# Kernel tuning notes

Measured on AMD Instinct MI355X. Metric: run time of the kernel, lower is better.

Reference implementation:

```python
import jax, jax.numpy as jnp
import numpy as np

B = 32            # decode batch (N flat tokens, q_len=1 each)
D_MODEL = 4096
H = 32            # query heads
HKV = 8           # kv heads (GQA)
HD = 128          # head dim
KVLEN = 2048      # context length per sequence
BLOCK = 256       # paged-cache block size
NBPS = KVLEN // BLOCK          # blocks per sequence = 8
NBLOCKS = B * NBPS             # 256
NSLOTS = NBLOCKS * BLOCK       # 65536
EPS = 1e-6
THETA = 10000.0
NEG = -1e30


def setup_inputs() -> dict:
    key = jax.random.key(0)
    ks = jax.random.split(key, 8)
    seqs = jax.random.normal(ks[0], (B, D_MODEL), dtype=jnp.float32)
    Wq = jax.random.normal(ks[1], (D_MODEL, H * HD), dtype=jnp.float32) * 0.02
    Wk = jax.random.normal(ks[2], (D_MODEL, HKV * HD), dtype=jnp.float32) * 0.02
    Wv = jax.random.normal(ks[3], (D_MODEL, HKV * HD), dtype=jnp.float32) * 0.02
    Wo = jax.random.normal(ks[4], (H * HD, D_MODEL), dtype=jnp.float32) * 0.02
    qn_w = jnp.ones((HD,), dtype=jnp.float32)
    kn_w = jnp.ones((HD,), dtype=jnp.float32)
    k_cache = jax.random.normal(ks[5], (NSLOTS, HKV, HD), dtype=jnp.float32) * 0.02
    v_cache = jax.random.normal(ks[6], (NSLOTS, HKV, HD), dtype=jnp.float32) * 0.02
    # decode step: each seq owns NBPS contiguous blocks; new token goes to last slot
    input_pos = jnp.full((B,), KVLEN - 1, dtype=jnp.int32)
    slot_mapping = (jnp.arange(B, dtype=jnp.int32) * NBPS * BLOCK + (KVLEN - 1)).astype(jnp.int32)
    block_tables = jnp.arange(NBLOCKS, dtype=jnp.int32).reshape(B, NBPS)
    context_lens = jnp.full((B,), KVLEN, dtype=jnp.int32)
    return {
        'seqs': seqs, 'Wq': Wq, 'Wk': Wk, 'Wv': Wv, 'Wo': Wo,
        'qn_w': qn_w, 'kn_w': kn_w, 'k_cache': k_cache, 'v_cache': v_cache,
        'input_pos': input_pos, 'slot_mapping': slot_mapping,
        'block_tables': block_tables, 'context_lens': context_lens,
    }


def _rmsnorm(x, w):
    return x * jax.lax.rsqrt(jnp.mean(x * x, axis=-1, keepdims=True) + EPS) * w


def _rope(x, pos):
    # x: [N, heads, HD], pos: [N]
    half = HD // 2
    inv = 1.0 / (THETA ** (jnp.arange(half, dtype=jnp.float32) / half))
    ang = pos.astype(jnp.float32)[:, None] * inv          # [N, half]
    cos = jnp.cos(ang)[:, None, :]
    sin = jnp.sin(ang)[:, None, :]
    x1, x2 = x[..., :half], x[..., half:]
    return jnp.concatenate([x1 * cos - x2 * sin, x2 * cos + x1 * sin], axis=-1)


def reference(seqs, Wq, Wk, Wv, Wo, qn_w, kn_w, k_cache, v_cache,
              input_pos, slot_mapping, block_tables, context_lens):
    # QKV projections (flat token layout, N = B decode tokens)
    q = (seqs @ Wq).reshape(B, H, HD)
    k = (seqs @ Wk).reshape(B, HKV, HD)
    v = (seqs @ Wv).reshape(B, HKV, HD)
    # qk-norm then RoPE
    q = _rmsnorm(q, qn_w)
    k = _rmsnorm(k, kn_w)
    q = _rope(q, input_pos)
    k = _rope(k, input_pos)
    # paged KV-cache store (slot_mapping scatter)
    kc = k_cache.at[slot_mapping].set(k)
    vc = v_cache.at[slot_mapping].set(v)
    # block-table-indexed gather: slots per sequence [B, KVLEN]
    slots = (block_tables[:, :, None] * BLOCK
             + jnp.arange(BLOCK, dtype=jnp.int32)[None, None, :]).reshape(B, -1)
    K = kc[slots]   # [B, L, HKV, HD]
    V = vc[slots]   # [B, L, HKV, HD]
    L = slots.shape[1]
    # GQA attention: group query heads over kv heads
    G = H // HKV
    qg = q.reshape(B, HKV, G, HD)
    scale = 1.0 / jnp.sqrt(jnp.float32(HD))
    scores = jnp.einsum('bkgd,blkd->bkgl', qg, K) * scale   # [B, HKV, G, L]
    valid = jnp.arange(L, dtype=jnp.int32)[None, :] < context_lens[:, None]
    scores = jnp.where(valid[:, None, None, :], scores, NEG)
    p = jax.nn.softmax(scores, axis=-1)
    out = jnp.einsum('bkgl,blkd->bkgd', p, V).reshape(B, H * HD)
    return out @ Wo
```

## Files before the change

kernel.cpp:

```cpp
#include <hip/hip_runtime.h>
#include <hip/hip_bf16.h>
#include <math.h>

#define B_     32
#define DM_    4096
#define H_     32
#define HKV_   8
#define G_     4
#define HD_    128
#define KVLEN_ 2048
#define PBLK_  256
#define NBPS_  8
#define NQKV_  6144
#define KSPLIT_ 16
#define KC_    256

__global__ __launch_bounds__(256) void qkv_gemm(
    const float* __restrict__ seqs, const float* __restrict__ Wq,
    const float* __restrict__ Wk, const float* __restrict__ Wv,
    float* __restrict__ P1) {
  const int tid = threadIdx.x;
  const int nid = blockIdx.x % 24;
  const int kid = blockIdx.x / 24;
  const int k0 = kid * KC_;

  __shared__ __align__(16) float sT[KC_ * 36];
  #pragma unroll
  for (int m = 0; m < 32; ++m)
    sT[tid * 36 + m] = seqs[m * DM_ + k0 + tid];
  __syncthreads();

  const int n = nid * 256 + tid;
  const float* W; int col, ldw;
  if (nid < 16)      { W = Wq; col = n;        ldw = 4096; }
  else if (nid < 20) { W = Wk; col = n - 4096; ldw = 1024; }
  else               { W = Wv; col = n - 5120; ldw = 1024; }

  float acc[32];
  #pragma unroll
  for (int m = 0; m < 32; ++m) acc[m] = 0.f;

  const float* wp = W + (size_t)k0 * ldw + col;
  #pragma unroll 4
  for (int kk = 0; kk < KC_; ++kk) {
    float w = wp[(size_t)kk * ldw];
    const float4* s4 = (const float4*)&sT[kk * 36];
    #pragma unroll
    for (int mq = 0; mq < 8; ++mq) {
      float4 a = s4[mq];
      acc[mq * 4 + 0] = fmaf(a.x, w, acc[mq * 4 + 0]);
      acc[mq * 4 + 1] = fmaf(a.y, w, acc[mq * 4 + 1]);
      acc[mq * 4 + 2] = fmaf(a.z, w, acc[mq * 4 + 2]);
      acc[mq * 4 + 3] = fmaf(a.w, w, acc[mq * 4 + 3]);
    }
  }
  float* o = P1 + (size_t)kid * 32 * NQKV_ + n;
  #pragma unroll
  for (int m = 0; m < 32; ++m) o[(size_t)m * NQKV_] = acc[m];
}

__global__ __launch_bounds__(128) void reduce_norm_rope(
    const float* __restrict__ P1, const float* __restrict__ qn_w,
    const float* __restrict__ kn_w, const int* __restrict__ input_pos,
    float* __restrict__ qf, float* __restrict__ knew, float* __restrict__ vnew) {
  const int b = blockIdx.x / 48;
  const int hh = blockIdx.x % 48;
  const int tid = threadIdx.x;

  int col0, kind;
  if (hh < 32)      { kind = 0; col0 = hh * 128; }
  else if (hh < 40) { kind = 1; col0 = 4096 + (hh - 32) * 128; }
  else              { kind = 2; col0 = 5120 + (hh - 40) * 128; }

  float x = 0.f;
  const float* p = P1 + (size_t)b * NQKV_ + col0 + tid;
  #pragma unroll
  for (int s = 0; s < KSPLIT_; ++s) x += p[(size_t)s * 32 * NQKV_];

  if (kind == 2) {
    vnew[(size_t)b * 1024 + (hh - 40) * 128 + tid] = x;
    return;
  }

  __shared__ float lds[128];
  __shared__ float wred[2];
  float ss = x * x;
  #pragma unroll
  for (int off = 32; off > 0; off >>= 1) ss += __shfl_down(ss, off);
  if ((tid & 63) == 0) wred[tid >> 6] = ss;
  __syncthreads();
  float tot = wred[0] + wred[1];
  float r = rsqrtf(tot * (1.f / 128.f) + 1e-6f);
  const float* wv = (kind == 0) ? qn_w : kn_w;
  x = x * r * wv[tid];

  lds[tid] = x;
  __syncthreads();

  if (tid < 64) {
    float pos = (float)input_pos[b];
    float inv = powf(10000.f, -(float)tid * (1.f / 64.f));
    float ang = pos * inv;
    float c = cosf(ang), s = sinf(ang);
    float x1 = lds[tid], x2 = lds[tid + 64];
    float o1 = x1 * c - x2 * s;
    float o2 = x2 * c + x1 * s;
    float* dst = (kind == 0) ? (qf + (size_t)b * 4096 + hh * 128)
                             : (knew + (size_t)b * 1024 + (hh - 32) * 128);
    dst[tid] = o1;
    dst[tid + 64] = o2;
  }
}

__global__ __launch_bounds__(512) void attn_decode(
    const float* __restrict__ qf, const float* __restrict__ knew,
    const float* __restrict__ vnew, const float* __restrict__ kc,
    const float* __restrict__ vc, const int* __restrict__ block_tables,
    const int* __restrict__ slot_mapping, const int* __restrict__ context_lens,
    float* __restrict__ attn) {
  const int b   = blockIdx.x >> 3;
  const int kv  = blockIdx.x & 7;
  const int tid = threadIdx.x;
  const int lane = tid & 63;
  const int wid  = tid >> 6;
  const int l16  = lane & 15;
  const int gid  = tid >> 4;
  const int d0   = l16 * 8;

  const int ctx   = context_lens[b];
  const int fslot = slot_mapping[b];
  const int* bt   = block_tables + b * NBPS_;

  const float scale = 0.08838834764831845f;
  float q[4][8];
  #pragma unroll
  for (int g = 0; g < 4; ++g) {
    const float4* qp = (const float4*)(qf + ((size_t)b * H_ + kv * G_ + g) * HD_ + d0);
    float4 a = qp[0], c = qp[1];
    q[g][0] = a.x * scale; q[g][1] = a.y * scale; q[g][2] = a.z * scale; q[g][3] = a.w * scale;
    q[g][4] = c.x * scale; q[g][5] = c.y * scale; q[g][6] = c.z * scale; q[g][7] = c.w * scale;
  }

  float mx[4], ls[4], acc[4][8];
  #pragma unroll
  for (int g = 0; g < 4; ++g) {
    mx[g] = -1e30f; ls[g] = 0.f;
    #pragma unroll
    for (int j = 0; j < 8; ++j) acc[g][j] = 0.f;
  }

  for (int l = gid; l < ctx; l += 32) {
    int page = bt[l >> 8];
    int slot = (page << 8) + (l & 255);
    const float *kp, *vp;
    if (slot == fslot) {
      kp = knew + ((size_t)b * HKV_ + kv) * HD_;
      vp = vnew + ((size_t)b * HKV_ + kv) * HD_;
    } else {
      kp = kc + ((size_t)slot * HKV_ + kv) * HD_;
      vp = vc + ((size_t)slot * HKV_ + kv) * HD_;
    }
    float4 k1 = ((const float4*)(kp + d0))[0];
    float4 k2 = ((const float4*)(kp + d0))[1];
    float4 v1 = ((const float4*)(vp + d0))[0];
    float4 v2 = ((const float4*)(vp + d0))[1];
    float kk[8] = {k1.x, k1.y, k1.z, k1.w, k2.x, k2.y, k2.z, k2.w};
    float vv[8] = {v1.x, v1.y, v1.z, v1.w, v2.x, v2.y, v2.z, v2.w};

    float s[4];
    #pragma unroll
    for (int g = 0; g < 4; ++g) {
      float t = 0.f;
      #pragma unroll
      for (int j = 0; j < 8; ++j) t = fmaf(q[g][j], kk[j], t);
      s[g] = t;
    }
    #pragma unroll
    for (int off = 1; off < 16; off <<= 1) {
      #pragma unroll
      for (int g = 0; g < 4; ++g) s[g] += __shfl_xor(s[g], off);
    }
    #pragma unroll
    for (int g = 0; g < 4; ++g) {
      float nm = fmaxf(mx[g], s[g]);
      float corr = __expf(mx[g] - nm);
      float pw = __expf(s[g] - nm);
      mx[g] = nm;
      ls[g] = ls[g] * corr + pw;
      #pragma unroll
      for (int j = 0; j < 8; ++j) acc[g][j] = fmaf(acc[g][j], corr, pw * vv[j]);
    }
  }

  #pragma unroll
  for (int off = 16; off < 64; off <<= 1) {
    #pragma unroll
    for (int g = 0; g < 4; ++g) {
      float mo = __shfl_xor(mx[g], off);
      float lo = __shfl_xor(ls[g], off);
      float nm = fmaxf(mx[g], mo);
      float c1 = __expf(mx[g] - nm);
      float c2 = __expf(mo - nm);
      ls[g] = ls[g] * c1 + lo * c2;
      mx[g] = nm;
      #pragma unroll
      for (int j = 0; j < 8; ++j) {
        float ao = __shfl_xor(acc[g][j], off);
        acc[g][j] = acc[g][j] * c1 + ao * c2;
      }
    }
  }

  __shared__ float rm[8][4], rl[8][4];
  __shared__ __align__(16) float ra[8][4][128];
  if (lane < 16) {
    #pragma unroll
    for (int g = 0; g < 4; ++g) {
      #pragma unroll
      for (int j = 0; j < 8; ++j) ra[wid][g][d0 + j] = acc[g][j];
    }
    if (lane == 0) {
      #pragma unroll
      for (int g = 0; g < 4; ++g) { rm[wid][g] = mx[g]; rl[wid][g] = ls[g]; }
    }
  }
  __syncthreads();

  {
    int g = tid >> 7;
    int d = tid & 127;
    float M = -1e30f;
    #pragma unroll
    for (int w = 0; w < 8; ++w) M = fmaxf(M, rm[w][g]);
    float L = 0.f, A = 0.f;
    #pragma unroll
    for (int w = 0; w < 8; ++w) {
      float c = __expf(rm[w][g] - M);
      L += c * rl[w][g];
      A += c * ra[w][g][d];
    }
    attn[((size_t)b * H_ + kv * G_ + g) * HD_ + d] = A / L;
  }
}

__global__ __launch_bounds__(256) void oproj_gemm(
    const float* __restrict__ A, const float* __restrict__ Wo,
    float* __restrict__ P2) {
  const int tid = threadIdx.x;
  const int nid = blockIdx.x & 15;
  const int kid = blockIdx.x >> 4;
  const int k0 = kid * KC_;

  __shared__ __align__(16) float sT[KC_ * 36];
  #pragma unroll
  for (int m = 0; m < 32; ++m)
    sT[tid * 36 + m] = A[m * 4096 + k0 + tid];
  __syncthreads();

  const int n = nid * 256 + tid;
  float acc[32];
  #pragma unroll
  for (int m = 0; m < 32; ++m) acc[m] = 0.f;

  const float* wp = Wo + (size_t)k0 * 4096 + n;
  #pragma unroll 4
  for (int kk = 0; kk < KC_; ++kk) {
    float w = wp[(size_t)kk * 4096];
    const float4* s4 = (const float4*)&sT[kk * 36];
    #pragma unroll
    for (int mq = 0; mq < 8; ++mq) {
      float4 a = s4[mq];
      acc[mq * 4 + 0] = fmaf(a.x, w, acc[mq * 4 + 0]);
      acc[mq * 4 + 1] = fmaf(a.y, w, acc[mq * 4 + 1]);
      acc[mq * 4 + 2] = fmaf(a.z, w, acc[mq * 4 + 2]);
      acc[mq * 4 + 3] = fmaf(a.w, w, acc[mq * 4 + 3]);
    }
  }
  float* o = P2 + (size_t)kid * 32 * 4096 + n;
  #pragma unroll
  for (int m = 0; m < 32; ++m) o[(size_t)m * 4096] = acc[m];
}

__global__ __launch_bounds__(256) void oproj_reduce(
    const float* __restrict__ P2, float* __restrict__ out) {
  const int idx = blockIdx.x * 256 + threadIdx.x;
  float s = 0.f;
  #pragma unroll
  for (int t = 0; t < KSPLIT_; ++t) s += P2[(size_t)t * 131072 + idx];
  out[idx] = s;
}

extern "C" void kernel_launch(void* const* d_in, const int* in_sizes, int n_in,
                              void* d_out, int out_size, void* d_ws, size_t ws_size,
                              hipStream_t stream) {
  const float* seqs = (const float*)d_in[0];
  const float* Wq   = (const float*)d_in[1];
  const float* Wk   = (const float*)d_in[2];
  const float* Wv   = (const float*)d_in[3];
  const float* Wo   = (const float*)d_in[4];
  const float* qn_w = (const float*)d_in[5];
  const float* kn_w = (const float*)d_in[6];
  const float* kc   = (const float*)d_in[7];
  const float* vc   = (const float*)d_in[8];
  const int* input_pos = (const int*)d_in[9];
  const int* slot_map  = (const int*)d_in[10];
  const int* btab      = (const int*)d_in[11];
  const int* ctx       = (const int*)d_in[12];
  float* out = (float*)d_out;

  char* w = (char*)d_ws;
  float* P1   = (float*)(w);
  float* qf   = (float*)(w + 12582912);
  float* knew = (float*)(w + 13107200);
  float* vnew = (float*)(w + 13238272);
  float* attn = (float*)(w + 13369344);
  float* P2   = (float*)(w + 13893632);

  qkv_gemm<<<24 * KSPLIT_, 256, 0, stream>>>(seqs, Wq, Wk, Wv, P1);
  reduce_norm_rope<<<B_ * 48, 128, 0, stream>>>(P1, qn_w, kn_w, input_pos, qf, knew, vnew);
  attn_decode<<<B_ * HKV_, 512, 0, stream>>>(qf, knew, vnew, kc, vc, btab, slot_map, ctx, attn);
  oproj_gemm<<<16 * KSPLIT_, 256, 0, stream>>>(attn, Wo, P2);
  oproj_reduce<<<512, 256, 0, stream>>>(P2, out);
}
```

Baseline: 228.2 us.

## Split attention over context with max-free softmax merge and widen GEMM column loads

```diff
diff --git a/kernel.cpp b/kernel.cpp
--- a/kernel.cpp
+++ b/kernel.cpp
@@ -9,11 +9,12 @@
 #define G_     4
 #define HD_    128
 #define KVLEN_ 2048
-#define PBLK_  256
 #define NBPS_  8
 #define NQKV_  6144
 #define KSPLIT_ 16
 #define KC_    256
+#define ASPLIT_ 16
+#define APOS_  128
 
 __global__ __launch_bounds__(256) void qkv_gemm(
     const float* __restrict__ seqs, const float* __restrict__ Wq,
@@ -30,33 +31,46 @@
     sT[tid * 36 + m] = seqs[m * DM_ + k0 + tid];
   __syncthreads();
 
-  const int n = nid * 256 + tid;
+  const int ct = tid & 127;
+  const int mh = tid >> 7;
+  const int n  = nid * 256 + ct * 2;
+
   const float* W; int col, ldw;
   if (nid < 16)      { W = Wq; col = n;        ldw = 4096; }
   else if (nid < 20) { W = Wk; col = n - 4096; ldw = 1024; }
   else               { W = Wv; col = n - 5120; ldw = 1024; }
 
-  float acc[32];
-  #pragma unroll
-  for (int m = 0; m < 32; ++m) acc[m] = 0.f;
-
-  const float* wp = W + (size_t)k0 * ldw + col;
+  float2 acc[16];
+  #pragma unroll
+  for (int r = 0; r < 16; ++r) acc[r] = make_float2(0.f, 0.f);
+
+  const float2* wp = (const float2*)(W + (size_t)k0 * ldw + col);
+  const int ldw2 = ldw >> 1;
+
   #pragma unroll 4
   for (int kk = 0; kk < KC_; ++kk) {
-    float w = wp[(size_t)kk * ldw];
-    const float4* s4 = (const float4*)&sT[kk * 36];
-    #pragma unroll
-    for (int mq = 0; mq < 8; ++mq) {
-      float4 a = s4[mq];
-      acc[mq * 4 + 0] = fmaf(a.x, w, acc[mq * 4 + 0]);
-      acc[mq * 4 + 1] = fmaf(a.y, w, acc[mq * 4 + 1]);
-      acc[mq * 4 + 2] = fmaf(a.z, w, acc[mq * 4 + 2]);
-      acc[mq * 4 + 3] = fmaf(a.w, w, acc[mq * 4 + 3]);
-    }
-  }
+    float2 w = wp[(size_t)kk * ldw2];
+    const float4* s4 = (const float4*)(sT + kk * 36 + mh * 16);
+    #pragma unroll
+    for (int rq = 0; rq < 4; ++rq) {
+      float4 a = s4[rq];
+      acc[rq*4+0].x = fmaf(a.x, w.x, acc[rq*4+0].x);
+      acc[rq*4+0].y = fmaf(a.x, w.y, acc[rq*4+0].y);
+      acc[rq*4+1].x = fmaf(a.y, w.x, acc[rq*4+1].x);
+      acc[rq*4+1].y = fmaf(a.y, w.y, acc[rq*4+1].y);
+      acc[rq*4+2].x = fmaf(a.z, w.x, acc[rq*4+2].x);
+      acc[rq*4+2].y = fmaf(a.z, w.y, acc[rq*4+2].y);
+      acc[rq*4+3].x = fmaf(a.w, w.x, acc[rq*4+3].x);
+      acc[rq*4+3].y = fmaf(a.w, w.y, acc[rq*4+3].y);
+    }
+  }
+
   float* o = P1 + (size_t)kid * 32 * NQKV_ + n;
   #pragma unroll
-  for (int m = 0; m < 32; ++m) o[(size_t)m * NQKV_] = acc[m];
+  for (int r = 0; r < 16; ++r) {
+    int m = mh * 16 + r;
+    *(float2*)(o + (size_t)m * NQKV_) = acc[r];
+  }
 }
 
 __global__ __launch_bounds__(128) void reduce_norm_rope(
@@ -117,130 +131,122 @@
     const float* __restrict__ vnew, const float* __restrict__ kc,
     const float* __restrict__ vc, const int* __restrict__ block_tables,
     const int* __restrict__ slot_mapping, const int* __restrict__ context_lens,
-    float* __restrict__ attn) {
-  const int b   = blockIdx.x >> 3;
-  const int kv  = blockIdx.x & 7;
+    float* __restrict__ pacc, float* __restrict__ pls) {
+  const int b   = blockIdx.x >> 4;
+  const int sp  = blockIdx.x & 15;
   const int tid = threadIdx.x;
+  const int w   = tid >> 6;
   const int lane = tid & 63;
-  const int wid  = tid >> 6;
-  const int l16  = lane & 15;
-  const int gid  = tid >> 4;
-  const int d0   = l16 * 8;
+  const int gi  = lane >> 4;
+  const int l16 = lane & 15;
+  const int d0  = l16 * 8;
 
   const int ctx   = context_lens[b];
   const int fslot = slot_mapping[b];
-  const int* bt   = block_tables + b * NBPS_;
+  const int base  = sp * APOS_;
+
+  const int page  = block_tables[b * NBPS_ + (base >> 8)];
+  const int slot0 = (page << 8) + (base & 255);
 
   const float scale = 0.08838834764831845f;
   float q[4][8];
   #pragma unroll
   for (int g = 0; g < 4; ++g) {
-    const float4* qp = (const float4*)(qf + ((size_t)b * H_ + kv * G_ + g) * HD_ + d0);
+    const float4* qp = (const float4*)(qf + ((size_t)b * H_ + w * G_ + g) * HD_ + d0);
     float4 a = qp[0], c = qp[1];
     q[g][0] = a.x * scale; q[g][1] = a.y * scale; q[g][2] = a.z * scale; q[g][3] = a.w * scale;
     q[g][4] = c.x * scale; q[g][5] = c.y * scale; q[g][6] = c.z * scale; q[g][7] = c.w * scale;
   }
 
-  float mx[4], ls[4], acc[4][8];
-  #pragma unroll
-  for (int g = 0; g < 4; ++g) {
-    mx[g] = -1e30f; ls[g] = 0.f;
+  const float* knp = knew + ((size_t)b * HKV_ + w) * HD_ + d0;
+  const float* vnp = vnew + ((size_t)b * HKV_ + w) * HD_ + d0;
+  const float* kcb = kc + ((size_t)slot0 * HKV_ + w) * HD_ + d0;
+  const float* vcb = vc + ((size_t)slot0 * HKV_ + w) * HD_ + d0;
+
+  float ls[4] = {0.f, 0.f, 0.f, 0.f};
+  float acc[4][8];
+  #pragma unroll
+  for (int g = 0; g < 4; ++g)
     #pragma unroll
     for (int j = 0; j < 8; ++j) acc[g][j] = 0.f;
-  }
-
-  for (int l = gid; l < ctx; l += 32) {
-    int page = bt[l >> 8];
-    int slot = (page << 8) + (l & 255);
-    const float *kp, *vp;
-    if (slot == fslot) {
-      kp = knew + ((size_t)b * HKV_ + kv) * HD_;
-      vp = vnew + ((size_t)b * HKV_ + kv) * HD_;
-    } else {
-      kp = kc + ((size_t)slot * HKV_ + kv) * HD_;
-      vp = vc + ((size_t)slot * HKV_ + kv) * HD_;
-    }
-    float4 k1 = ((const float4*)(kp + d0))[0];
-    float4 k2 = ((const float4*)(kp + d0))[1];
-    float4 v1 = ((const float4*)(vp + d0))[0];
-    float4 v2 = ((const float4*)(vp + d0))[1];
-    float kk[8] = {k1.x, k1.y, k1.z, k1.w, k2.x, k2.y, k2.z, k2.w};
-    float vv[8] = {v1.x, v1.y, v1.z, v1.w, v2.x, v2.y, v2.z, v2.w};
-
-    float s[4];
+
+  for (int it = 0; it < APOS_ / 4; ++it) {
+    const int off = it * 4 + gi;
+    const int pos = base + off;
+    if (pos < ctx) {
+      const int slot = slot0 + off;
+      const float* kp = (slot == fslot) ? knp : (kcb + (size_t)off * (HKV_ * HD_));
+      const float* vp = (slot == fslot) ? vnp : (vcb + (size_t)off * (HKV_ * HD_));
+      float4 k1 = ((const float4*)kp)[0];
+      float4 k2 = ((const float4*)kp)[1];
+      float4 v1 = ((const float4*)vp)[0];
+      float4 v2 = ((const float4*)vp)[1];
+      float kk8[8] = {k1.x, k1.y, k1.z, k1.w, k2.x, k2.y, k2.z, k2.w};
+      float vv[8]  = {v1.x, v1.y, v1.z, v1.w, v2.x, v2.y, v2.z, v2.w};
+
+      float s[4];
+      #pragma unroll
+      for (int g = 0; g < 4; ++g) {
+        float t = 0.f;
+        #pragma unroll
+        for (int j = 0; j < 8; ++j) t = fmaf(q[g][j], kk8[j], t);
+        s[g] = t;
+      }
+      #pragma unroll
+      for (int o2 = 1; o2 < 16; o2 <<= 1) {
+        #pragma unroll
+        for (int g = 0; g < 4; ++g) s[g] += __shfl_xor(s[g], o2);
+      }
+      #pragma unroll
+      for (int g = 0; g < 4; ++g) {
+        float pw = __expf(s[g]);
+        ls[g] += pw;
+        #pragma unroll
+        for (int j = 0; j < 8; ++j) acc[g][j] = fmaf(pw, vv[j], acc[g][j]);
+      }
+    }
+  }
+
+  #pragma unroll
+  for (int o2 = 16; o2 < 64; o2 <<= 1) {
     #pragma unroll
     for (int g = 0; g < 4; ++g) {
-      float t = 0.f;
+      ls[g] += __shfl_xor(ls[g], o2);
       #pragma unroll
-      for (int j = 0; j < 8; ++j) t = fmaf(q[g][j], kk[j], t);
-      s[g] = t;
-    }
-    #pragma unroll
-    for (int off = 1; off < 16; off <<= 1) {
-      #pragma unroll
-      for (int g = 0; g < 4; ++g) s[g] += __shfl_xor(s[g], off);
-    }
+      for (int j = 0; j < 8; ++j) acc[g][j] += __shfl_xor(acc[g][j], o2);
+    }
+  }
+
+  if (gi == 0) {
     #pragma unroll
     for (int g = 0; g < 4; ++g) {
-      float nm = fmaxf(mx[g], s[g]);
-      float corr = __expf(mx[g] - nm);
-      float pw = __expf(s[g] - nm);
-      mx[g] = nm;
-      ls[g] = ls[g] * corr + pw;
-      #pragma unroll
-      for (int j = 0; j < 8; ++j) acc[g][j] = fmaf(acc[g][j], corr, pw * vv[j]);
-    }
-  }
-
-  #pragma unroll
-  for (int off = 16; off < 64; off <<= 1) {
-    #pragma unroll
-    for (int g = 0; g < 4; ++g) {
-      float mo = __shfl_xor(mx[g], off);
-      float lo = __shfl_xor(ls[g], off);
-      float nm = fmaxf(mx[g], mo);
-      float c1 = __expf(mx[g] - nm);
-      float c2 = __expf(mo - nm);
-      ls[g] = ls[g] * c1 + lo * c2;
-      mx[g] = nm;
-      #pragma unroll
-      for (int j = 0; j < 8; ++j) {
-        float ao = __shfl_xor(acc[g][j], off);
-        acc[g][j] = acc[g][j] * c1 + ao * c2;
-      }
-    }
-  }
-
-  __shared__ float rm[8][4], rl[8][4];
-  __shared__ __align__(16) float ra[8][4][128];
-  if (lane < 16) {
-    #pragma unroll
-    for (int g = 0; g < 4; ++g) {
-      #pragma unroll
-      for (int j = 0; j < 8; ++j) ra[wid][g][d0 + j] = acc[g][j];
-    }
-    if (lane == 0) {
-      #pragma unroll
-      for (int g = 0; g < 4; ++g) { rm[wid][g] = mx[g]; rl[wid][g] = ls[g]; }
-    }
-  }
-  __syncthreads();
-
-  {
-    int g = tid >> 7;
-    int d = tid & 127;
-    float M = -1e30f;
-    #pragma unroll
-    for (int w = 0; w < 8; ++w) M = fmaxf(M, rm[w][g]);
-    float L = 0.f, A = 0.f;
-    #pragma unroll
-    for (int w = 0; w < 8; ++w) {
-      float c = __expf(rm[w][g] - M);
-      L += c * rl[w][g];
-      A += c * ra[w][g][d];
-    }
-    attn[((size_t)b * H_ + kv * G_ + g) * HD_ + d] = A / L;
-  }
+      float* dst = pacc + (((size_t)sp * B_ + b) * H_ + (w * G_ + g)) * HD_ + d0;
+      float4 o1 = {acc[g][0], acc[g][1], acc[g][2], acc[g][3]};
+      float4 o2 = {acc[g][4], acc[g][5], acc[g][6], acc[g][7]};
+      ((float4*)dst)[0] = o1;
+      ((float4*)dst)[1] = o2;
+      if (l16 == 0) pls[((size_t)sp * B_ + b) * H_ + (w * G_ + g)] = ls[g];
+    }
+  }
+}
+
+__global__ __launch_bounds__(256) void attn_merge(
+    const float* __restrict__ pacc, const float* __restrict__ pls,
+    float* __restrict__ attnb) {
+  const int idx = blockIdx.x * 256 + threadIdx.x;
+  const int bh  = idx >> 5;
+  const float4* p4 = (const float4*)pacc;
+  float4 A = {0.f, 0.f, 0.f, 0.f};
+  float L = 0.f;
+  #pragma unroll
+  for (int sp = 0; sp < ASPLIT_; ++sp) {
+    float4 t = p4[(size_t)sp * 32768 + idx];
+    A.x += t.x; A.y += t.y; A.z += t.z; A.w += t.w;
+    L += pls[sp * (B_ * H_) + bh];
+  }
+  float r = 1.f / L;
+  A.x *= r; A.y *= r; A.z *= r; A.w *= r;
+  ((float4*)attnb)[idx] = A;
 }
 
 __global__ __launch_bounds__(256) void oproj_gemm(
@@ -257,28 +263,40 @@
     sT[tid * 36 + m] = A[m * 4096 + k0 + tid];
   __syncthreads();
 
-  const int n = nid * 256 + tid;
-  float acc[32];
-  #pragma unroll
-  for (int m = 0; m < 32; ++m) acc[m] = 0.f;
-
-  const float* wp = Wo + (size_t)k0 * 4096 + n;
+  const int ct = tid & 127;
+  const int mh = tid >> 7;
+  const int n  = nid * 256 + ct * 2;
+
+  float2 acc[16];
+  #pragma unroll
+  for (int r = 0; r < 16; ++r) acc[r] = make_float2(0.f, 0.f);
+
+  const float2* wp = (const float2*)(Wo + (size_t)k0 * 4096 + n);
+
   #pragma unroll 4
   for (int kk = 0; kk < KC_; ++kk) {
-    float w = wp[(size_t)kk * 4096];
-    const float4* s4 = (const float4*)&sT[kk * 36];
-    #pragma unroll
-    for (int mq = 0; mq < 8; ++mq) {
-      float4 a = s4[mq];
-      acc[mq * 4 + 0] = fmaf(a.x, w, acc[mq * 4 + 0]);
-      acc[mq * 4 + 1] = fmaf(a.y, w, acc[mq * 4 + 1]);
-      acc[mq * 4 + 2] = fmaf(a.z, w, acc[mq * 4 + 2]);
-      acc[mq * 4 + 3] = fmaf(a.w, w, acc[mq * 4 + 3]);
-    }
-  }
+    float2 w = wp[(size_t)kk * 2048];
+    const float4* s4 = (const float4*)(sT + kk * 36 + mh * 16);
+    #pragma unroll
+    for (int rq = 0; rq < 4; ++rq) {
+      float4 a = s4[rq];
+      acc[rq*4+0].x = fmaf(a.x, w.x, acc[rq*4+0].x);
+      acc[rq*4+0].y = fmaf(a.x, w.y, acc[rq*4+0].y);
+      acc[rq*4+1].x = fmaf(a.y, w.x, acc[rq*4+1].x);
+      acc[rq*4+1].y = fmaf(a.y, w.y, acc[rq*4+1].y);
+      acc[rq*4+2].x = fmaf(a.z, w.x, acc[rq*4+2].x);
+      acc[rq*4+2].y = fmaf(a.z, w.y, acc[rq*4+2].y);
+      acc[rq*4+3].x = fmaf(a.w, w.x, acc[rq*4+3].x);
+      acc[rq*4+3].y = fmaf(a.w, w.y, acc[rq*4+3].y);
+    }
+  }
+
   float* o = P2 + (size_t)kid * 32 * 4096 + n;
   #pragma unroll
-  for (int m = 0; m < 32; ++m) o[(size_t)m * 4096] = acc[m];
+  for (int r = 0; r < 16; ++r) {
+    int m = mh * 16 + r;
+    *(float2*)(o + (size_t)m * 4096) = acc[r];
+  }
 }
 
 __global__ __launch_bounds__(256) void oproj_reduce(
@@ -309,16 +327,19 @@
   float* out = (float*)d_out;
 
   char* w = (char*)d_ws;
-  float* P1   = (float*)(w);
-  float* qf   = (float*)(w + 12582912);
-  float* knew = (float*)(w + 13107200);
-  float* vnew = (float*)(w + 13238272);
-  float* attn = (float*)(w + 13369344);
-  float* P2   = (float*)(w + 13893632);
+  float* P1    = (float*)(w);
+  float* qf    = (float*)(w + 12582912);
+  float* knew  = (float*)(w + 13107200);
+  float* vnew  = (float*)(w + 13238272);
+  float* attnb = (float*)(w + 13369344);
+  float* pacc  = (float*)(w + 13893632);
+  float* pls   = (float*)(w + 22282240);
+  float* P2    = (float*)(w + 22347776);
 
   qkv_gemm<<<24 * KSPLIT_, 256, 0, stream>>>(seqs, Wq, Wk, Wv, P1);
   reduce_norm_rope<<<B_ * 48, 128, 0, stream>>>(P1, qn_w, kn_w, input_pos, qf, knew, vnew);
-  attn_decode<<<B_ * HKV_, 512, 0, stream>>>(qf, knew, vnew, kc, vc, btab, slot_map, ctx, attn);
-  oproj_gemm<<<16 * KSPLIT_, 256, 0, stream>>>(attn, Wo, P2);
+  attn_decode<<<B_ * ASPLIT_, 512, 0, stream>>>(qf, knew, vnew, kc, vc, btab, slot_map, ctx, pacc, pls);
+  attn_merge<<<128, 256, 0, stream>>>(pacc, pls, attnb);
+  oproj_gemm<<<16 * KSPLIT_, 256, 0, stream>>>(attnb, Wo, P2);
   oproj_reduce<<<512, 256, 0, stream>>>(P2, out);
 }
```

Result: faster. 211.8 us (-7.2%).
